# Performance work log

Measured on AMD Instinct MI355X. Metric: run time of the kernel, lower is better.

The kernel has to match this reference:

```python
import jax, jax.numpy as jnp
import numpy as np

IN_BIT = 8      # in_bit_width
W_BIT = 2       # weight_bit_width (also output act quantizer bit width)
BN_EPS = 1e-4


def _ste(x, q):
    # straight-through estimator: forward = q, backward = identity w.r.t. x
    return x + jax.lax.stop_gradient(q - x)


def act_quant(x, bit):
    # CommonActQuant: signed int quant, narrow_range=False, power-of-two scale
    # range [-1, 1 - 2^{-(bit-1)}] -> scale = 2^{-(bit-1)}
    s = 2.0 ** (1 - bit)
    n_min = -(2.0 ** (bit - 1))
    n_max = 2.0 ** (bit - 1) - 1.0
    q = jnp.clip(jnp.round(x / s), n_min, n_max) * s
    return _ste(x, q)


def weight_quant(w, bit):
    # CommonWeightQuant: narrow-range signed int quant, unit scaling const
    # scale = 1 / (2^{bit-1} - 1); for bit=2 levels are {-1, 0, 1}
    n = 2.0 ** (bit - 1) - 1.0
    s = 1.0 / n
    q = jnp.clip(jnp.round(w / s), -n, n) * s
    return _ste(w, q)


def setup_inputs() -> dict:
    key = jax.random.key(0)
    k1, k2, k3, k4 = jax.random.split(key, 4)
    B, C, H, W = 32, 256, 32, 32
    x = jax.random.normal(k1, (B, C, H, W), dtype=jnp.float32) * 0.5
    weight = jax.random.normal(k2, (C, C, 3, 3), dtype=jnp.float32) * 0.5
    gamma = jnp.ones((C,), dtype=jnp.float32)
    beta = jnp.zeros((C,), dtype=jnp.float32)
    running_mean = jax.random.normal(k3, (C,), dtype=jnp.float32) * 0.1
    running_var = jax.random.uniform(k4, (C,), dtype=jnp.float32, minval=0.5, maxval=1.5)
    return {"x": x, "weight": weight, "gamma": gamma, "beta": beta,
            "running_mean": running_mean, "running_var": running_var}


def reference(x, weight, gamma, beta, running_mean, running_var):
    # 1) input QuantIdentity (8-bit, [-1, 1-2^-7], power-of-two scale 2^-7)
    xq = act_quant(x, IN_BIT)
    # 2) QuantConv2d 3x3 stride 1 pad 1, no bias, 2-bit weights
    wq = weight_quant(weight, W_BIT)
    y = jax.lax.conv_general_dilated(
        xq, wq, window_strides=(1, 1), padding=((1, 1), (1, 1)),
        dimension_numbers=("NCHW", "OIHW", "NCHW"))
    # 3) BatchNorm2d (inference, eps=1e-4)
    inv = gamma / jnp.sqrt(running_var + BN_EPS)
    y = y * inv[None, :, None, None] + (beta - running_mean * inv)[None, :, None, None]
    # 4) output QuantIdentity at weight_bit_width bits
    return act_quant(y, W_BIT)
```

## Files before the change

### kernel.cpp

```cpp
#include <hip/hip_runtime.h>
#include <hip/hip_bf16.h>
#include <stdint.h>


typedef int i32x4 __attribute__((ext_vector_type(4)));
typedef float f32x4 __attribute__((ext_vector_type(4)));

__device__ __forceinline__ void gload_lds16(const void* g, const void* lds_byte_ptr) {
    __builtin_amdgcn_global_load_lds(
        (const __attribute__((address_space(1))) unsigned int*)(uintptr_t)g,
        (__attribute__((address_space(3))) unsigned int*)(uintptr_t)lds_byte_ptr,
        16, 0, 0);
}

__global__ __launch_bounds__(256) void quant_w_kernel(const float* __restrict__ w,
                                                      signed char* __restrict__ wq) {
    __shared__ signed char tile[2304];
    const int co = blockIdx.x;
    const int t = threadIdx.x;
#pragma unroll
    for (int p = 0; p < 9; ++p) {
        const int idx = p * 256 + t;
        const float v = w[co * 2304 + idx];
        const int ci = idx / 9;
        const int khkw = idx - 9 * ci;
        const float q = fminf(fmaxf(rintf(v), -1.f), 1.f);
        tile[khkw * 256 + ci] = (signed char)(int)q;
    }
    __syncthreads();
    if (t < 144) {
        *(uint4*)(wq + (size_t)co * 2304 + t * 16) = *(const uint4*)(tile + t * 16);
    }
}

__global__ __launch_bounds__(256) void quant_x_kernel(const float* __restrict__ x,
                                                      signed char* __restrict__ xpad) {
    __shared__ signed char tile[32 * 272];
    const int t = threadIdx.x;
    const int b = blockIdx.x >> 5;
    const int h = blockIdx.x & 31;
    const int w = t & 31;
    const int cg = (t >> 5) * 4;
#pragma unroll
    for (int p = 0; p < 8; ++p) {
        const int ci = p * 32 + cg;
        unsigned packed = 0;
#pragma unroll
        for (int k = 0; k < 4; ++k) {
            const float v = x[(((size_t)(b * 256 + ci + k)) * 32 + h) * 32 + w];
            float q = fminf(fmaxf(rintf(__fmul_rn(v, 128.f)), -128.f), 127.f);
            packed |= ((unsigned)(unsigned char)(signed char)(int)q) << (8 * k);
        }
        *(unsigned*)(tile + w * 272 + ci) = packed;
    }
    __syncthreads();
#pragma unroll
    for (int q = 0; q < 2; ++q) {
        const int wp = q * 16 + (t >> 4);
        const int ci16 = (t & 15) * 16;
        uint4 v = *(const uint4*)(tile + wp * 272 + ci16);
        *(uint4*)(xpad + (size_t)(((b * 34 + h + 1) * 34) + (wp + 1)) * 256 + ci16) = v;
    }
}

__global__ __launch_bounds__(256) void conv_gemm_kernel(
    const signed char* __restrict__ xpad, const signed char* __restrict__ wq,
    const float* __restrict__ gamma, const float* __restrict__ beta,
    const float* __restrict__ mean, const float* __restrict__ var,
    float* __restrict__ out)
{
    __shared__ signed char As[128 * 64];
    __shared__ signed char Bs[128 * 64];

    const int tid = threadIdx.x;
    const int wv = tid >> 6;
    const int lane = tid & 63;
    const int quad = lane >> 4;
    const int l16 = lane & 15;

    const int m0 = (blockIdx.x >> 1) * 128;
    const int n0 = (blockIdx.x & 1) * 128;
    const int wave_m = wv & 1;
    const int wave_n = wv >> 1;

    i32x4 acc[4][4];
#pragma unroll
    for (int i = 0; i < 4; i++)
#pragma unroll
        for (int j = 0; j < 4; j++) acc[i][j] = (i32x4){0, 0, 0, 0};

    for (int kt = 0; kt < 36; ++kt) {
        const int khkw = kt >> 2;
        const int kh = khkw / 3;
        const int kw = khkw - 3 * kh;
        const int ci0 = (kt & 3) * 64;
#pragma unroll
        for (int s = 0; s < 2; ++s) {
            const int row = s * 64 + wv * 16 + (lane >> 2);
            const int cic = (lane & 3) * 16;
            const unsigned ldsOff = (unsigned)(s * 4096 + wv * 1024);
            const int m = m0 + row;
            const int b = m >> 10;
            const int h = (m >> 5) & 31;
            const int w = m & 31;
            const signed char* ga =
                xpad + (size_t)(((b * 34 + h + kh) * 34) + (w + kw)) * 256 + ci0 + cic;
            gload_lds16(ga, As + ldsOff);
            const signed char* gb = wq + (size_t)(n0 + row) * 2304 + kt * 64 + cic;
            gload_lds16(gb, Bs + ldsOff);
        }
        __syncthreads();

        i32x4 af[4], bfr[4];
#pragma unroll
        for (int i = 0; i < 4; i++) {
            const int row = wave_m * 64 + i * 16 + l16;
            af[i] = *(const i32x4*)(As + row * 64 + quad * 16);
        }
#pragma unroll
        for (int j = 0; j < 4; j++) {
            const int row = wave_n * 64 + j * 16 + l16;
            bfr[j] = *(const i32x4*)(Bs + row * 64 + quad * 16);
        }
#pragma unroll
        for (int i = 0; i < 4; i++)
#pragma unroll
            for (int j = 0; j < 4; j++)
                acc[i][j] = __builtin_amdgcn_mfma_i32_16x16x64_i8(af[i], bfr[j], acc[i][j], 0, 0, 0);
        __syncthreads();
    }

#pragma unroll
    for (int j = 0; j < 4; j++) {
        const int co = n0 + wave_n * 64 + j * 16 + l16;
        const float iv = __fdiv_rn(gamma[co], __fsqrt_rn(__fadd_rn(var[co], 1e-4f)));
        const float bias = __fsub_rn(beta[co], __fmul_rn(mean[co], iv));
#pragma unroll
        for (int i = 0; i < 4; i++) {
            const int m_base = m0 + wave_m * 64 + i * 16 + quad * 4;
            const int b = m_base >> 10;
            const int h = (m_base >> 5) & 31;
            const int w = m_base & 31;
            f32x4 v;
#pragma unroll
            for (int r = 0; r < 4; r++) {
                const float y = __fmul_rn((float)acc[i][j][r], 0.0078125f);
                const float t = __fadd_rn(__fmul_rn(y, iv), bias);
                float z = rintf(__fmul_rn(t, 2.f));
                z = fminf(fmaxf(z, -2.f), 1.f);
                v[r] = __fmul_rn(z, 0.5f);
            }
            *(f32x4*)(&out[(((size_t)(b * 256 + co)) * 32 + h) * 32 + w]) = v;
        }
    }
}

extern "C" void kernel_launch(void* const* d_in, const int* in_sizes, int n_in,
                              void* d_out, int out_size, void* d_ws, size_t ws_size,
                              hipStream_t stream) {
    const float* x      = (const float*)d_in[0];
    const float* weight = (const float*)d_in[1];
    const float* gamma  = (const float*)d_in[2];
    const float* beta   = (const float*)d_in[3];
    const float* rmean  = (const float*)d_in[4];
    const float* rvar   = (const float*)d_in[5];
    float* out = (float*)d_out;

    signed char* wq   = (signed char*)d_ws;
    signed char* xpad = (signed char*)d_ws + (1 << 20);

    quant_w_kernel<<<256, 256, 0, stream>>>(weight, wq);
    hipMemsetAsync(xpad, 0, (size_t)32 * 34 * 34 * 256, stream);
    quant_x_kernel<<<1024, 256, 0, stream>>>(x, xpad);
    conv_gemm_kernel<<<512, 256, 0, stream>>>(xpad, wq, gamma, beta, rmean, rvar, out);
}
```

Measured before the change: 126.8 us.

## Zero padding inside quant_x and split conv block across eight waves

The quantize-x kernel now also writes the zero halo rows and columns itself, so the full-buffer memset before it is dropped. The conv GEMM block moves from 4 waves to 8 waves (512 threads), each wave computing a 64x32 output sub-tile with half the accumulators. Each thread now issues one global-to-LDS load per operand per k-step instead of two. This cuts per-wave register pressure and adds latency hiding, at the cost of more MFMA fragment reloads of A from LDS and more threads waiting at each barrier.

```diff
diff --git a/kernel.cpp b/kernel.cpp
--- a/kernel.cpp
+++ b/kernel.cpp
@@ -37,8 +37,15 @@
                                                       signed char* __restrict__ xpad) {
     __shared__ signed char tile[32 * 272];
     const int t = threadIdx.x;
-    const int b = blockIdx.x >> 5;
-    const int h = blockIdx.x & 31;
+    const int b = blockIdx.x / 34;
+    const int hp = blockIdx.x % 34;
+    signed char* rowbase = xpad + (size_t)((b * 34 + hp) * 34) * 256;
+    const uint4 z = {0u, 0u, 0u, 0u};
+    if (hp == 0 || hp == 33) {
+        for (int i = t; i < 544; i += 256) *(uint4*)(rowbase + i * 16) = z;
+        return;
+    }
+    const int h = hp - 1;
     const int w = t & 31;
     const int cg = (t >> 5) * 4;
 #pragma unroll
@@ -59,11 +66,15 @@
         const int wp = q * 16 + (t >> 4);
         const int ci16 = (t & 15) * 16;
         uint4 v = *(const uint4*)(tile + wp * 272 + ci16);
-        *(uint4*)(xpad + (size_t)(((b * 34 + h + 1) * 34) + (wp + 1)) * 256 + ci16) = v;
+        *(uint4*)(rowbase + (size_t)(wp + 1) * 256 + ci16) = v;
+    }
+    if (t < 32) {
+        const int wp = (t >> 4) * 33;
+        *(uint4*)(rowbase + (size_t)wp * 256 + (t & 15) * 16) = z;
     }
 }
 
-__global__ __launch_bounds__(256) void conv_gemm_kernel(
+__global__ __launch_bounds__(512) void conv_gemm_kernel(
     const signed char* __restrict__ xpad, const signed char* __restrict__ wq,
     const float* __restrict__ gamma, const float* __restrict__ beta,
     const float* __restrict__ mean, const float* __restrict__ var,
@@ -83,56 +94,53 @@
     const int wave_m = wv & 1;
     const int wave_n = wv >> 1;
 
-    i32x4 acc[4][4];
+    i32x4 acc[4][2];
 #pragma unroll
     for (int i = 0; i < 4; i++)
 #pragma unroll
-        for (int j = 0; j < 4; j++) acc[i][j] = (i32x4){0, 0, 0, 0};
+        for (int j = 0; j < 2; j++) acc[i][j] = (i32x4){0, 0, 0, 0};
+
+    const int srow = tid >> 2;
+    const int scic = (tid & 3) * 16;
+    const unsigned ldsOff = (unsigned)(wv * 1024);
+    const int sb = (m0 + srow) >> 10;
+    const int sh = ((m0 + srow) >> 5) & 31;
+    const int sw = (m0 + srow) & 31;
 
     for (int kt = 0; kt < 36; ++kt) {
         const int khkw = kt >> 2;
         const int kh = khkw / 3;
         const int kw = khkw - 3 * kh;
         const int ci0 = (kt & 3) * 64;
-#pragma unroll
-        for (int s = 0; s < 2; ++s) {
-            const int row = s * 64 + wv * 16 + (lane >> 2);
-            const int cic = (lane & 3) * 16;
-            const unsigned ldsOff = (unsigned)(s * 4096 + wv * 1024);
-            const int m = m0 + row;
-            const int b = m >> 10;
-            const int h = (m >> 5) & 31;
-            const int w = m & 31;
-            const signed char* ga =
-                xpad + (size_t)(((b * 34 + h + kh) * 34) + (w + kw)) * 256 + ci0 + cic;
-            gload_lds16(ga, As + ldsOff);
-            const signed char* gb = wq + (size_t)(n0 + row) * 2304 + kt * 64 + cic;
-            gload_lds16(gb, Bs + ldsOff);
-        }
+        const signed char* ga =
+            xpad + (size_t)(((sb * 34 + sh + kh) * 34) + (sw + kw)) * 256 + ci0 + scic;
+        gload_lds16(ga, As + ldsOff);
+        const signed char* gb = wq + (size_t)(n0 + srow) * 2304 + kt * 64 + scic;
+        gload_lds16(gb, Bs + ldsOff);
         __syncthreads();
 
-        i32x4 af[4], bfr[4];
+        i32x4 af[4], bfr[2];
 #pragma unroll
         for (int i = 0; i < 4; i++) {
             const int row = wave_m * 64 + i * 16 + l16;
             af[i] = *(const i32x4*)(As + row * 64 + quad * 16);
         }
 #pragma unroll
-        for (int j = 0; j < 4; j++) {
-            const int row = wave_n * 64 + j * 16 + l16;
+        for (int j = 0; j < 2; j++) {
+            const int row = wave_n * 32 + j * 16 + l16;
             bfr[j] = *(const i32x4*)(Bs + row * 64 + quad * 16);
         }
 #pragma unroll
         for (int i = 0; i < 4; i++)
 #pragma unroll
-            for (int j = 0; j < 4; j++)
+            for (int j = 0; j < 2; j++)
                 acc[i][j] = __builtin_amdgcn_mfma_i32_16x16x64_i8(af[i], bfr[j], acc[i][j], 0, 0, 0);
         __syncthreads();
     }
 
 #pragma unroll
-    for (int j = 0; j < 4; j++) {
-        const int co = n0 + wave_n * 64 + j * 16 + l16;
+    for (int j = 0; j < 2; j++) {
+        const int co = n0 + wave_n * 32 + j * 16 + l16;
         const float iv = __fdiv_rn(gamma[co], __fsqrt_rn(__fadd_rn(var[co], 1e-4f)));
         const float bias = __fsub_rn(beta[co], __fmul_rn(mean[co], iv));
 #pragma unroll
@@ -170,7 +178,6 @@
     signed char* xpad = (signed char*)d_ws + (1 << 20);
 
     quant_w_kernel<<<256, 256, 0, stream>>>(weight, wq);
-    hipMemsetAsync(xpad, 0, (size_t)32 * 34 * 34 * 256, stream);
-    quant_x_kernel<<<1024, 256, 0, stream>>>(x, xpad);
-    conv_gemm_kernel<<<512, 256, 0, stream>>>(xpad, wq, gamma, beta, rmean, rvar, out);
+    quant_x_kernel<<<1088, 256, 0, stream>>>(x, xpad);
+    conv_gemm_kernel<<<512, 512, 0, stream>>>(xpad, wq, gamma, beta, rmean, rvar, out);
 }
```

After: 123.5 us. 1.03x faster.
